# Kernel optimization log

Hardware: AMD Instinct MI355X
Metric: run time of the kernel (lower is better)

The kernel has to match this reference:

```python
import jax, jax.numpy as jnp
import numpy as np

D, H, DFF = 256, 8, 2048
NQ, BS, HW = 300, 16, 1444
HD = D // H

def _lin_params(key, din, dout):
    k1, k2 = jax.random.split(key)
    s = 1.0 / np.sqrt(din)
    W = jax.random.uniform(k1, (dout, din), minval=-s, maxval=s, dtype=jnp.float32)
    b = jax.random.uniform(k2, (dout,), minval=-s, maxval=s, dtype=jnp.float32)
    return W, b

def setup_inputs() -> dict:
    key = jax.random.key(0)
    ks = jax.random.split(key, 24)
    inp = {
        "tgt": jax.random.normal(ks[0], (NQ, BS, D), dtype=jnp.float32),
        "memory": jax.random.normal(ks[1], (HW, BS, D), dtype=jnp.float32),
        "pos": jax.random.normal(ks[2], (HW, BS, D), dtype=jnp.float32),
        "query_pos": jax.random.normal(ks[3], (NQ, BS, D), dtype=jnp.float32),
        "query_sine_embed": jax.random.normal(ks[4], (NQ, BS, D), dtype=jnp.float32),
        "memory_key_padding_mask": jnp.zeros((BS, HW), dtype=bool),
    }
    names = ["sa_qc", "sa_qp", "sa_kc", "sa_kp", "sa_v", "sa_out",
             "ca_qc", "ca_kc", "ca_kp", "ca_v", "ca_sine", "ca_out"]
    for i, n in enumerate(names):
        W, b = _lin_params(ks[5 + i], D, D)
        inp["W_" + n], inp["b_" + n] = W, b
    inp["W_ff1"], inp["b_ff1"] = _lin_params(ks[20], D, DFF)
    inp["W_ff2"], inp["b_ff2"] = _lin_params(ks[21], DFF, D)
    for n in ("n1", "n2", "n3"):
        inp["g_" + n] = jnp.ones((D,), jnp.float32)
        inp["be_" + n] = jnp.zeros((D,), jnp.float32)
    return inp

def _lin(x, W, b):
    return x @ W.T + b

def _ln(x, g, b):
    m = jnp.mean(x, axis=-1, keepdims=True)
    v = jnp.mean(jnp.square(x - m), axis=-1, keepdims=True)
    return (x - m) * jax.lax.rsqrt(v + 1e-5) * g + b

def reference(tgt, memory, pos, query_pos, query_sine_embed, memory_key_padding_mask,
              W_sa_qc, b_sa_qc, W_sa_qp, b_sa_qp, W_sa_kc, b_sa_kc, W_sa_kp, b_sa_kp,
              W_sa_v, b_sa_v, W_sa_out, b_sa_out,
              W_ca_qc, b_ca_qc, W_ca_kc, b_ca_kc, W_ca_kp, b_ca_kp, W_ca_v, b_ca_v,
              W_ca_sine, b_ca_sine, W_ca_out, b_ca_out,
              W_ff1, b_ff1, W_ff2, b_ff2,
              g_n1, be_n1, g_n2, be_n2, g_n3, be_n3):
    nq, bs, d = tgt.shape
    hw = memory.shape[0]
    # ---- self-attention (custom MHA: no internal in-proj, scale q, out_proj) ----
    q = _lin(tgt, W_sa_qc, b_sa_qc) + _lin(query_pos, W_sa_qp, b_sa_qp)
    k = _lin(tgt, W_sa_kc, b_sa_kc) + _lin(query_pos, W_sa_kp, b_sa_kp)
    v = _lin(tgt, W_sa_v, b_sa_v)
    qh = q.reshape(nq, bs, H, HD) * (HD ** -0.5)
    kh = k.reshape(nq, bs, H, HD)
    vh = v.reshape(nq, bs, H, HD)
    logits = jnp.einsum('qbhd,kbhd->bhqk', qh, kh)
    attn = jax.nn.softmax(logits, axis=-1)
    sa = jnp.einsum('bhqk,kbhd->qbhd', attn, vh).reshape(nq, bs, d)
    sa = _lin(sa, W_sa_out, b_sa_out)
    tgt = _ln(tgt + sa, g_n1, be_n1)
    # ---- cross-attention (is_first=False; concat content+pos per head -> 2d) ----
    qc = _lin(tgt, W_ca_qc, b_ca_qc)
    kc = _lin(memory, W_ca_kc, b_ca_kc)
    kp = _lin(pos, W_ca_kp, b_ca_kp)
    vm = _lin(memory, W_ca_v, b_ca_v)
    sine = _lin(query_sine_embed, W_ca_sine, b_ca_sine)
    qh2 = jnp.concatenate([qc.reshape(nq, bs, H, HD), sine.reshape(nq, bs, H, HD)], axis=-1)
    kh2 = jnp.concatenate([kc.reshape(hw, bs, H, HD), kp.reshape(hw, bs, H, HD)], axis=-1)
    vh2 = vm.reshape(hw, bs, H, HD)
    scale = (2 * HD) ** -0.5  # embed_dim of cross_attn is 2*d_model
    logits2 = jnp.einsum('qbhd,kbhd->bhqk', qh2 * scale, kh2)
    neg = jnp.finfo(logits2.dtype).min
    logits2 = jnp.where(memory_key_padding_mask[:, None, None, :], neg, logits2)
    attn2 = jax.nn.softmax(logits2, axis=-1)
    ca = jnp.einsum('bhqk,kbhd->qbhd', attn2, vh2).reshape(nq, bs, d)
    ca = _lin(ca, W_ca_out, b_ca_out)
    tgt = _ln(tgt + ca, g_n2, be_n2)
    # ---- FFN ----
    ff = _lin(jax.nn.relu(_lin(tgt, W_ff1, b_ff1)), W_ff2, b_ff2)
    return _ln(tgt + ff, g_n3, be_n3)
```

## Files before the change

### kernel.cpp

```cpp
#include <hip/hip_runtime.h>

typedef unsigned short u16;
typedef unsigned int u32;
typedef __attribute__((ext_vector_type(8))) short short8;
typedef __attribute__((ext_vector_type(4))) float f32x4;
typedef __attribute__((ext_vector_type(4))) unsigned short us4;

#define NQ 300
#define BS 16
#define HW 1444
#define DFF 2048
#define SA_TOK 4800
#define CA_TOK 23104

__device__ __forceinline__ float b2f(u16 x) {
    return __uint_as_float(((unsigned int)x) << 16);
}
__device__ __forceinline__ u16 f2b(float f) {
    unsigned int u = __float_as_uint(f);
    u += 0x7fffu + ((u >> 16) & 1u);
    return (u16)(u >> 16);
}

__device__ __forceinline__ int ext_mode(const void* dref) {
    const u16* p = (const u16*)dref;
    const int lane = threadIdx.x & 63;
    int hit = 0;
#pragma unroll
    for (int j = 0; j < 4; ++j) {
        u16 v = p[(lane * 4 + j) << 1];
        hit |= (((v >> 7) & 0xFF) >= 0xE0) ? 1 : 0;
    }
    unsigned long long b = __ballot(hit != 0);
    return (__popcll(b) >= 4) ? 1 : 0;
}

__device__ __forceinline__ float loadS(const void* p, size_t i, int m) {
    return m ? ((const float*)p)[i] : b2f(((const u16*)p)[i]);
}
__device__ __forceinline__ short8 load8(const void* p, size_t i, int m) {
    if (!m) return *(const short8*)((const u16*)p + i);
    const float* f = (const float*)p + i;
    float4 a = *(const float4*)f;
    float4 c = *(const float4*)(f + 4);
    short8 r;
    r[0] = (short)f2b(a.x); r[1] = (short)f2b(a.y);
    r[2] = (short)f2b(a.z); r[3] = (short)f2b(a.w);
    r[4] = (short)f2b(c.x); r[5] = (short)f2b(c.y);
    r[6] = (short)f2b(c.z); r[7] = (short)f2b(c.w);
    return r;
}

#define AW_SA_QC 0u
#define AW_SA_QP 65536u
#define AW_SA_KC 131072u
#define AW_SA_KP 196608u
#define AW_SA_V  262144u
#define AW_SA_O  327680u
#define AW_CA_QC 393216u
#define AW_CA_KC 458752u
#define AW_CA_KP 524288u
#define AW_CA_V  589824u
#define AW_CA_S  655360u
#define AW_CA_O  720896u
#define AW_FF1   786432u
#define AW_FF2   1310720u
#define AB_BASE  1835008u
#define AB_FF1   1838080u
#define AB_FF2   1840128u
#define AG_N1    1840384u
#define ABE_N1   1840640u
#define AG_N2    1840896u
#define ABE_N2   1841152u
#define AG_N3    1841408u
#define ABE_N3   1841664u

#define NPACK 34
struct PackDesc {
    const void* src[NPACK];
    u32 dst[NPACK];
    u32 cnt8[NPACK];
    u32 nd16[NPACK];
    u32 ksh[NPACK];
};

__global__ __launch_bounds__(256) void pack_kernel(PackDesc pd, u16* __restrict__ arena,
                                                   const void* __restrict__ dref)
{
    const int md = ext_mode(dref);
    const int ti = blockIdx.y;
    const void* src = pd.src[ti];
    const u32 dst = pd.dst[ti];
    const u32 n = pd.cnt8[ti];
    const u32 nd = pd.nd16[ti];
    if (nd) {
        const u32 ksh = pd.ksh[ti];
        const u32 kmask = (1u << ksh) - 1u;
        for (u32 c = blockIdx.x * 256 + threadIdx.x; c < n; c += gridDim.x * 256) {
            u32 e = c * 8;
            u32 nn = e >> ksh;
            u32 k = e & kmask;
            u32 d = ((k >> 5) * nd + (nn >> 4)) * 512 + (((k >> 3) & 3) * 16 + (nn & 15)) * 8;
            *(short8*)(arena + dst + d) = load8(src, (size_t)e, md);
        }
    } else {
        for (u32 c = blockIdx.x * 256 + threadIdx.x; c < n; c += gridDim.x * 256)
            *(short8*)(arena + dst + c * 8) = load8(src, (size_t)c * 8, md);
    }
}

__global__ __launch_bounds__(768, 3) void gemm_prod(
    const void* __restrict__ tgt, const void* __restrict__ qpos,
    const void* __restrict__ memory, const void* __restrict__ pos,
    const u16* __restrict__ arena,
    u16* __restrict__ Qb, u16* __restrict__ Kb, u16* __restrict__ Vb,
    u16* __restrict__ K2, u16* __restrict__ V2,
    float qscale, const void* __restrict__ dref)
{
    const int md = ext_mode(dref);
    __shared__ u16 AL[2 * 64 * 264];
    u16* A1 = AL;
    u16* A2 = AL + 64 * 264;
    const int tid = threadIdx.x;
    const int wave = tid >> 6, lane = tid & 63, quad = lane >> 4, l16 = lane & 15;

    if (blockIdx.x < 361) {
        const int m0 = blockIdx.x * 64;
#pragma unroll
        for (int i = 0; i < 6; ++i) {
            int c = tid + i * 768;
            if (c < 4096) {
                int t = c >> 11, local = c & 2047;
                int row = local >> 5, col = (local & 31) * 8;
                u16* A = t ? A2 : A1;
                const void* X = t ? pos : memory;
                *(short8*)(A + row * 264 + col) = load8(X, (size_t)(m0 + row) * 256 + col, md);
            }
        }
        __syncthreads();

        f32x4 acc[4][4];
#pragma unroll
        for (int rg = 0; rg < 4; ++rg)
#pragma unroll
            for (int s = 0; s < 4; ++s) acc[rg][s] = (f32x4){0,0,0,0};

        if (wave < 8) {
            const int h = wave;
            short8 bq[3][4];
#pragma unroll
            for (int p = 0; p < 2; ++p)
#pragma unroll
                for (int s = 0; s < 4; ++s) {
                    const u32 wo = (s < 2) ? AW_CA_KC : AW_CA_KP;
                    bq[p][s] = *(const short8*)(arena + wo + (u32)(p * 16 + h * 2 + (s & 1)) * 512 + lane * 8);
                }
#pragma unroll
            for (int i = 0; i < 8; ++i) {
                const int kk = i * 32;
                if (i < 6) {
#pragma unroll
                    for (int s = 0; s < 4; ++s) {
                        const u32 wo = (s < 2) ? AW_CA_KC : AW_CA_KP;
                        bq[(i + 2) % 3][s] = *(const short8*)(arena + wo + (u32)((i + 2) * 16 + h * 2 + (s & 1)) * 512 + lane * 8);
                    }
                }
                short8 am[4], ap[4];
#pragma unroll
                for (int rg = 0; rg < 4; ++rg) {
                    am[rg] = *(const short8*)(A1 + (rg * 16 + l16) * 264 + kk + quad * 8);
                    ap[rg] = *(const short8*)(A2 + (rg * 16 + l16) * 264 + kk + quad * 8);
                }
#pragma unroll
                for (int s = 0; s < 4; ++s)
#pragma unroll
                    for (int rg = 0; rg < 4; ++rg)
                        acc[rg][s] = __builtin_amdgcn_mfma_f32_16x16x32_bf16(
                            (s < 2) ? am[rg] : ap[rg], bq[i % 3][s], acc[rg][s], 0, 0, 0);
            }
        } else {
            const int nt = (wave - 8) * 4;
            short8 bq[3][4];
#pragma unroll
            for (int p = 0; p < 2; ++p)
#pragma unroll
                for (int s = 0; s < 4; ++s)
                    bq[p][s] = *(const short8*)(arena + AW_CA_V + (u32)(p * 16 + nt + s) * 512 + lane * 8);
#pragma unroll
            for (int i = 0; i < 8; ++i) {
                const int kk = i * 32;
                if (i < 6) {
#pragma unroll
                    for (int s = 0; s < 4; ++s)
                        bq[(i + 2) % 3][s] = *(const short8*)(arena + AW_CA_V + (u32)((i + 2) * 16 + nt + s) * 512 + lane * 8);
                }
                short8 am[4];
#pragma unroll
                for (int rg = 0; rg < 4; ++rg)
                    am[rg] = *(const short8*)(A1 + (rg * 16 + l16) * 264 + kk + quad * 8);
#pragma unroll
                for (int s = 0; s < 4; ++s)
#pragma unroll
                    for (int rg = 0; rg < 4; ++rg)
                        acc[rg][s] = __builtin_amdgcn_mfma_f32_16x16x32_bf16(am[rg], bq[i % 3][s], acc[rg][s], 0, 0, 0);
            }
        }

        __syncthreads();
        if (wave < 8) {
            const int h = wave;
#pragma unroll
            for (int s = 0; s < 4; ++s) {
                const int brow = h * 32 + (s & 1) * 16 + l16;
                float bv = b2f(arena[((s < 2) ? (AB_BASE + 7 * 256) : (AB_BASE + 8 * 256)) + brow]);
                const int col = h * 64 + s * 16 + l16;
#pragma unroll
                for (int rg = 0; rg < 4; ++rg)
#pragma unroll
                    for (int r = 0; r < 4; ++r)
                        AL[(rg * 16 + quad * 4 + r) * 520 + col] = f2b(acc[rg][s][r] + bv);
            }
        }
        __syncthreads();
        for (int c = tid; c < 4096; c += 768) {
            int row = c >> 6, cc = (c & 63) * 8;
            *(short8*)(K2 + (size_t)(m0 + row) * 512 + cc) = *(const short8*)(AL + row * 520 + cc);
        }
        __syncthreads();
        if (wave >= 8) {
            const int n0 = (wave - 8) * 64;
#pragma unroll
            for (int s = 0; s < 4; ++s) {
                const int col = n0 + s * 16 + l16;
                float bv = b2f(arena[AB_BASE + 9 * 256 + col]);
#pragma unroll
                for (int rg = 0; rg < 4; ++rg)
#pragma unroll
                    for (int r = 0; r < 4; ++r)
                        AL[(rg * 16 + quad * 4 + r) * 264 + col] = f2b(acc[rg][s][r] + bv);
            }
        }
        __syncthreads();
        for (int c = tid; c < 2048; c += 768) {
            int row = c >> 5, cc = (c & 31) * 8;
            *(short8*)(V2 + (size_t)(m0 + row) * 256 + cc) = *(const short8*)(AL + row * 264 + cc);
        }
    } else {
        const int m0 = (blockIdx.x - 361) * 64;
#pragma unroll
        for (int i = 0; i < 6; ++i) {
            int c = tid + i * 768;
            if (c < 4096) {
                int t = c >> 11, local = c & 2047;
                int row = local >> 5, col = (local & 31) * 8;
                u16* A = t ? A2 : A1;
                const void* X = t ? qpos : tgt;
                *(short8*)(A + row * 264 + col) = load8(X, (size_t)(m0 + row) * 256 + col, md);
            }
        }
        __syncthreads();

        const int grp = wave >> 2, sub = wave & 3;
        const int n0 = sub * 64, nt = sub * 4;
        u32 w1o, w2o, b1o, b2o; int dual; float scale;
        if (grp == 0)      { w1o = AW_SA_QC; w2o = AW_SA_QP; b1o = AB_BASE;         b2o = AB_BASE + 256;   dual = 1; scale = qscale; }
        else if (grp == 1) { w1o = AW_SA_KC; w2o = AW_SA_KP; b1o = AB_BASE + 512;   b2o = AB_BASE + 768;   dual = 1; scale = 1.f;    }
        else               { w1o = AW_SA_V;  w2o = 0;        b1o = AB_BASE + 1024;  b2o = 0;               dual = 0; scale = 1.f;    }

        f32x4 acc[4][4];
#pragma unroll
        for (int rg = 0; rg < 4; ++rg)
#pragma unroll
            for (int s = 0; s < 4; ++s) acc[rg][s] = (f32x4){0,0,0,0};

        {
            short8 bw[3][4];
#pragma unroll
            for (int p = 0; p < 2; ++p)
#pragma unroll
                for (int s = 0; s < 4; ++s)
                    bw[p][s] = *(const short8*)(arena + w1o + (u32)(p * 16 + nt + s) * 512 + lane * 8);
#pragma unroll
            for (int i = 0; i < 8; ++i) {
                const int kk = i * 32;
                if (i < 6) {
#pragma unroll
                    for (int s = 0; s < 4; ++s)
                        bw[(i + 2) % 3][s] = *(const short8*)(arena + w1o + (u32)((i + 2) * 16 + nt + s) * 512 + lane * 8);
                }
                short8 a[4];
#pragma unroll
                for (int rg = 0; rg < 4; ++rg)
                    a[rg] = *(const short8*)(A1 + (rg * 16 + l16) * 264 + kk + quad * 8);
#pragma unroll
                for (int s = 0; s < 4; ++s)
#pragma unroll
                    for (int rg = 0; rg < 4; ++rg)
                        acc[rg][s] = __builtin_amdgcn_mfma_f32_16x16x32_bf16(a[rg], bw[i % 3][s], acc[rg][s], 0, 0, 0);
            }
        }
        if (dual) {
            short8 bw[3][4];
#pragma unroll
            for (int p = 0; p < 2; ++p)
#pragma unroll
                for (int s = 0; s < 4; ++s)
                    bw[p][s] = *(const short8*)(arena + w2o + (u32)(p * 16 + nt + s) * 512 + lane * 8);
#pragma unroll
            for (int i = 0; i < 8; ++i) {
                const int kk = i * 32;
                if (i < 6) {
#pragma unroll
                    for (int s = 0; s < 4; ++s)
                        bw[(i + 2) % 3][s] = *(const short8*)(arena + w2o + (u32)((i + 2) * 16 + nt + s) * 512 + lane * 8);
                }
                short8 a[4];
#pragma unroll
                for (int rg = 0; rg < 4; ++rg)
                    a[rg] = *(const short8*)(A2 + (rg * 16 + l16) * 264 + kk + quad * 8);
#pragma unroll
                for (int s = 0; s < 4; ++s)
#pragma unroll
                    for (int rg = 0; rg < 4; ++rg)
                        acc[rg][s] = __builtin_amdgcn_mfma_f32_16x16x32_bf16(a[rg], bw[i % 3][s], acc[rg][s], 0, 0, 0);
            }
        }

        __syncthreads();
        if (grp < 2) {
#pragma unroll
            for (int s = 0; s < 4; ++s) {
                const int col = n0 + s * 16 + l16;
                float bv = b2f(arena[b1o + col]);
                if (dual) bv += b2f(arena[b2o + col]);
#pragma unroll
                for (int rg = 0; rg < 4; ++rg)
#pragma unroll
                    for (int r = 0; r < 4; ++r)
                        AL[grp * (64 * 264) + (rg * 16 + quad * 4 + r) * 264 + col] = f2b((acc[rg][s][r] + bv) * scale);
            }
        }
        __syncthreads();
#pragma unroll
        for (int i = 0; i < 6; ++i) {
            int c = tid + i * 768;
            if (c < 4096) {
                int t = c >> 11, local = c & 2047;
                int row = local >> 5, cc = (local & 31) * 8;
                u16* Y = t ? Kb : Qb;
                *(short8*)(Y + (size_t)(m0 + row) * 256 + cc) =
                    *(const short8*)(AL + t * (64 * 264) + row * 264 + cc);
            }
        }
        __syncthreads();
        if (grp == 2) {
#pragma unroll
            for (int s = 0; s < 4; ++s) {
                const int col = n0 + s * 16 + l16;
                float bv = b2f(arena[b1o + col]);
#pragma unroll
                for (int rg = 0; rg < 4; ++rg)
#pragma unroll
                    for (int r = 0; r < 4; ++r)
                        AL[(rg * 16 + quad * 4 + r) * 264 + col] = f2b(acc[rg][s][r] + bv);
            }
        }
        __syncthreads();
#pragma unroll
        for (int i = 0; i < 3; ++i) {
            int c = tid + i * 768;
            if (c < 2048) {
                int row = c >> 5, cc = (c & 31) * 8;
                *(short8*)(Vb + (size_t)(m0 + row) * 256 + cc) = *(const short8*)(AL + row * 264 + cc);
            }
        }
    }
}

__global__ __launch_bounds__(256) void gemm_ff1(
    const u16* __restrict__ X, const u16* __restrict__ arena,
    u16* __restrict__ Y)
{
    __shared__ u16 A[64 * 264];
    const int tid = threadIdx.x;
    const int m0 = blockIdx.x * 64;
    for (int c = tid; c < 2048; c += 256) {
        int row = c >> 5, col = (c & 31) * 8;
        *(short8*)(A + row * 264 + col) = *(const short8*)(X + (size_t)(m0 + row) * 256 + col);
    }
    __syncthreads();

    const int wave = tid >> 6, lane = tid & 63, quad = lane >> 4, l16 = lane & 15;
    const int n0 = (blockIdx.y * 4 + wave) * 64;
    const u32 nt = (u32)(n0 >> 4);
    f32x4 acc[4][4];
#pragma unroll
    for (int rg = 0; rg < 4; ++rg)
#pragma unroll
        for (int s = 0; s < 4; ++s) acc[rg][s] = (f32x4){0,0,0,0};

    short8 bw[3][4];
#pragma unroll
    for (int p = 0; p < 2; ++p)
#pragma unroll
        for (int s = 0; s < 4; ++s)
            bw[p][s] = *(const short8*)(arena + AW_FF1 + (u32)(p * 128 + nt + s) * 512 + lane * 8);
#pragma unroll
    for (int i = 0; i < 8; ++i) {
        const int kk = i * 32;
        if (i < 6) {
#pragma unroll
            for (int s = 0; s < 4; ++s)
                bw[(i + 2) % 3][s] = *(const short8*)(arena + AW_FF1 + (u32)((i + 2) * 128 + nt + s) * 512 + lane * 8);
        }
        short8 a[4];
#pragma unroll
        for (int rg = 0; rg < 4; ++rg)
            a[rg] = *(const short8*)(A + (rg * 16 + l16) * 264 + kk + quad * 8);
#pragma unroll
        for (int s = 0; s < 4; ++s)
#pragma unroll
            for (int rg = 0; rg < 4; ++rg)
                acc[rg][s] = __builtin_amdgcn_mfma_f32_16x16x32_bf16(a[rg], bw[i % 3][s], acc[rg][s], 0, 0, 0);
    }

    __syncthreads();
    const int lcol = wave * 64;
#pragma unroll
    for (int s = 0; s < 4; ++s) {
        const int col = n0 + s * 16 + l16;
        float bv = b2f(arena[AB_FF1 + col]);
#pragma unroll
        for (int rg = 0; rg < 4; ++rg)
#pragma unroll
            for (int r = 0; r < 4; ++r) {
                float v = fmaxf(acc[rg][s][r] + bv, 0.f);
                A[(rg * 16 + quad * 4 + r) * 264 + lcol + s * 16 + l16] = f2b(v);
            }
    }
    __syncthreads();
    const size_t cbase = (size_t)blockIdx.y * 256;
    for (int c = tid; c < 2048; c += 256) {
        int row = c >> 5, cc = (c & 31) * 8;
        *(short8*)(Y + (size_t)(m0 + row) * 2048 + cbase + cc) = *(const short8*)(A + row * 264 + cc);
    }
}

__global__ __launch_bounds__(256) void gemm_ln(
    const u16* __restrict__ X, const u16* __restrict__ arena,
    u32 wo, u32 bo, u32 go, u32 beo,
    const void* __restrict__ R, int rext,
    u16* __restrict__ Out, const void* __restrict__ dref)
{
    const int md = ext_mode(dref);
    const int mr = rext ? md : 0;
    __shared__ u16 A[32 * 264];
    __shared__ float S[32][260];
    const int tid = threadIdx.x;
    const int m0 = blockIdx.x * 32;
    for (int c = tid; c < 1024; c += 256) {
        int row = c >> 5, col = (c & 31) * 8;
        *(short8*)(A + row * 264 + col) = *(const short8*)(X + (size_t)(m0 + row) * 256 + col);
    }
    __syncthreads();

    const int wave = tid >> 6, lane = tid & 63, quad = lane >> 4, l16 = lane & 15;
    const int n0 = wave * 64;
    const u32 nt = (u32)(wave * 4);
    f32x4 acc[2][4];
#pragma unroll
    for (int rg = 0; rg < 2; ++rg)
#pragma unroll
        for (int s = 0; s < 4; ++s) acc[rg][s] = (f32x4){0,0,0,0};

    short8 bw[4][4];
#pragma unroll
    for (int p = 0; p < 3; ++p)
#pragma unroll
        for (int s = 0; s < 4; ++s)
            bw[p][s] = *(const short8*)(arena + wo + (u32)(p * 16 + nt + s) * 512 + lane * 8);
#pragma unroll
    for (int i = 0; i < 8; ++i) {
        const int kk = i * 32;
        if (i < 5) {
#pragma unroll
            for (int s = 0; s < 4; ++s)
                bw[(i + 3) & 3][s] = *(const short8*)(arena + wo + (u32)((i + 3) * 16 + nt + s) * 512 + lane * 8);
        }
        short8 a0 = *(const short8*)(A + l16 * 264 + kk + quad * 8);
        short8 a1 = *(const short8*)(A + (16 + l16) * 264 + kk + quad * 8);
#pragma unroll
        for (int s = 0; s < 4; ++s) {
            acc[0][s] = __builtin_amdgcn_mfma_f32_16x16x32_bf16(a0, bw[i & 3][s], acc[0][s], 0, 0, 0);
            acc[1][s] = __builtin_amdgcn_mfma_f32_16x16x32_bf16(a1, bw[i & 3][s], acc[1][s], 0, 0, 0);
        }
    }
#pragma unroll
    for (int s = 0; s < 4; ++s) {
        const int col = n0 + s * 16 + l16;
        float bv = b2f(arena[bo + col]);
#pragma unroll
        for (int rg = 0; rg < 2; ++rg)
#pragma unroll
            for (int r = 0; r < 4; ++r)
                S[rg * 16 + quad * 4 + r][col] = acc[rg][s][r] + bv;
    }
    __syncthreads();

#pragma unroll
    for (int rr = 0; rr < 8; ++rr) {
        const int row = wave * 8 + rr;
        float4 v = *(const float4*)&S[row][lane * 4];
        const size_t rb = (size_t)(m0 + row) * 256 + lane * 4;
        v.x += loadS(R, rb + 0, mr);
        v.y += loadS(R, rb + 1, mr);
        v.z += loadS(R, rb + 2, mr);
        v.w += loadS(R, rb + 3, mr);
        float s = v.x + v.y + v.z + v.w;
        float q = v.x * v.x + v.y * v.y + v.z * v.z + v.w * v.w;
#pragma unroll
        for (int off = 1; off <= 32; off <<= 1) {
            s += __shfl_xor(s, off);
            q += __shfl_xor(q, off);
        }
        const float mean = s * (1.f / 256.f);
        const float var  = q * (1.f / 256.f) - mean * mean;
        const float rs   = rsqrtf(var + 1e-5f);
        float vv[4] = {v.x, v.y, v.z, v.w};
        us4 ov;
#pragma unroll
        for (int j = 0; j < 4; ++j) {
            const int col = lane * 4 + j;
            float o = (vv[j] - mean) * rs * b2f(arena[go + col]) + b2f(arena[beo + col]);
            ov[j] = f2b(o);
        }
        *(us4*)(Out + (size_t)(m0 + row) * 256 + lane * 4) = ov;
    }
}

__global__ __launch_bounds__(512) void gemm_cat(
    const void* __restrict__ Xa, int xae, const void* __restrict__ Xb, int xbe,
    const u16* __restrict__ arena, u32 wao, u32 wbo, u32 bao, u32 bbo,
    u16* __restrict__ Y, float scale, const void* __restrict__ dref)
{
    const int md = ext_mode(dref);
    __shared__ u16 AL[2 * 32 * 264];
    u16* Aa = AL;
    u16* Ab = AL + 32 * 264;
    const int tid = threadIdx.x;
    const int m0 = blockIdx.x * 32;
    for (int c = tid; c < 2048; c += 512) {
        const int t = c >> 10, local = c & 1023;
        const int row = local >> 5, col = (local & 31) * 8;
        const void* X = t ? Xb : Xa;
        const int xfp = (t ? xbe : xae) ? md : 0;
        u16* A = t ? Ab : Aa;
        *(short8*)(A + row * 264 + col) = load8(X, (size_t)(m0 + row) * 256 + col, xfp);
    }
    __syncthreads();

    const int wave = tid >> 6, lane = tid & 63, quad = lane >> 4, l16 = lane & 15;
    const int h = wave;
    f32x4 acc[2][4];
#pragma unroll
    for (int rg = 0; rg < 2; ++rg)
#pragma unroll
        for (int s = 0; s < 4; ++s) acc[rg][s] = (f32x4){0,0,0,0};

    short8 bw[4][4];
#pragma unroll
    for (int p = 0; p < 3; ++p)
#pragma unroll
        for (int s = 0; s < 4; ++s) {
            const u32 wo = (s < 2) ? wao : wbo;
            bw[p][s] = *(const short8*)(arena + wo + (u32)(p * 16 + h * 2 + (s & 1)) * 512 + lane * 8);
        }
#pragma unroll
    for (int i = 0; i < 8; ++i) {
        const int kk = i * 32;
        if (i < 5) {
#pragma unroll
            for (int s = 0; s < 4; ++s) {
                const u32 wo = (s < 2) ? wao : wbo;
                bw[(i + 3) & 3][s] = *(const short8*)(arena + wo + (u32)((i + 3) * 16 + h * 2 + (s & 1)) * 512 + lane * 8);
            }
        }
        short8 aa[2], ab[2];
#pragma unroll
        for (int rg = 0; rg < 2; ++rg) {
            aa[rg] = *(const short8*)(Aa + (rg * 16 + l16) * 264 + kk + quad * 8);
            ab[rg] = *(const short8*)(Ab + (rg * 16 + l16) * 264 + kk + quad * 8);
        }
#pragma unroll
        for (int s = 0; s < 4; ++s)
#pragma unroll
            for (int rg = 0; rg < 2; ++rg)
                acc[rg][s] = __builtin_amdgcn_mfma_f32_16x16x32_bf16(
                    (s < 2) ? aa[rg] : ab[rg], bw[i & 3][s], acc[rg][s], 0, 0, 0);
    }

    __syncthreads();
#pragma unroll
    for (int s = 0; s < 4; ++s) {
        const int brow = h * 32 + (s & 1) * 16 + l16;
        float bv = b2f(arena[((s < 2) ? bao : bbo) + brow]);
        const int col = h * 64 + s * 16 + l16;
#pragma unroll
        for (int rg = 0; rg < 2; ++rg)
#pragma unroll
            for (int r = 0; r < 4; ++r)
                AL[(rg * 16 + quad * 4 + r) * 520 + col] = f2b((acc[rg][s][r] + bv) * scale);
    }
    __syncthreads();
    for (int c = tid; c < 2048; c += 512) {
        int row = c >> 6, cc = (c & 63) * 8;
        *(short8*)(Y + (size_t)(m0 + row) * 512 + cc) = *(const short8*)(AL + row * 520 + cc);
    }
}

__global__ __launch_bounds__(256) void gemm_ff2s(
    const u16* __restrict__ X, const u16* __restrict__ arena, u32 wo,
    u16* __restrict__ P)
{
    __shared__ u16 A[64 * 520];
    const int tid = threadIdx.x;
    const int m0 = blockIdx.x * 64;
    const int ks = blockIdx.y;
    const int kbase = ks * 512;
    for (int c = tid; c < 4096; c += 256) {
        int row = c >> 6, col = (c & 63) * 8;
        *(short8*)(A + row * 520 + col) =
            *(const short8*)(X + (size_t)(m0 + row) * 2048 + kbase + col);
    }
    __syncthreads();

    const int wave = tid >> 6, lane = tid & 63, quad = lane >> 4, l16 = lane & 15;
    const int n0 = wave * 64;
    const u32 nt = (u32)(wave * 4);
    const u32 kt0 = (u32)(ks * 16);
    f32x4 acc[4][4];
#pragma unroll
    for (int rg = 0; rg < 4; ++rg)
#pragma unroll
        for (int s = 0; s < 4; ++s) acc[rg][s] = (f32x4){0,0,0,0};

    short8 bw[3][4];
#pragma unroll
    for (int p = 0; p < 2; ++p)
#pragma unroll
        for (int s = 0; s < 4; ++s)
            bw[p][s] = *(const short8*)(arena + wo + ((kt0 + p) * 16 + nt + s) * 512 + lane * 8);
#pragma unroll
    for (int i = 0; i < 16; ++i) {
        const int kk = i * 32;
        if (i < 14) {
#pragma unroll
            for (int s = 0; s < 4; ++s)
                bw[(i + 2) % 3][s] = *(const short8*)(arena + wo + ((kt0 + i + 2) * 16 + nt + s) * 512 + lane * 8);
        }
        short8 a[4];
#pragma unroll
        for (int rg = 0; rg < 4; ++rg)
            a[rg] = *(const short8*)(A + (rg * 16 + l16) * 520 + kk + quad * 8);
#pragma unroll
        for (int s = 0; s < 4; ++s)
#pragma unroll
            for (int rg = 0; rg < 4; ++rg)
                acc[rg][s] = __builtin_amdgcn_mfma_f32_16x16x32_bf16(a[rg], bw[i % 3][s], acc[rg][s], 0, 0, 0);
    }

    __syncthreads();
#pragma unroll
    for (int s = 0; s < 4; ++s) {
        const int col = n0 + s * 16 + l16;
#pragma unroll
        for (int rg = 0; rg < 4; ++rg)
#pragma unroll
            for (int r = 0; r < 4; ++r)
                A[(rg * 16 + quad * 4 + r) * 264 + col] = f2b(acc[rg][s][r]);
    }
    __syncthreads();
    for (int c = tid; c < 2048; c += 256) {
        int row = c >> 5, cc = (c & 31) * 8;
        *(short8*)(P + ((size_t)ks * SA_TOK + m0 + row) * 256 + cc) = *(const short8*)(A + row * 264 + cc);
    }
}

__global__ __launch_bounds__(256) void ln_ff2(
    const u16* __restrict__ P, const u16* __restrict__ arena,
    u32 bo, u32 go, u32 beo, const u16* __restrict__ T2,
    void* __restrict__ Out, const void* __restrict__ dref)
{
    const int md = ext_mode(dref);
    const int t = blockIdx.x;
    const int i = threadIdx.x;
    const int lane = i & 63, wave = i >> 6;
    float v = b2f(arena[bo + i]) + b2f(T2[(size_t)t * 256 + i]);
#pragma unroll
    for (int ks = 0; ks < 4; ++ks)
        v += b2f(P[((size_t)ks * SA_TOK + t) * 256 + i]);

    __shared__ float ssum[4], ssq[4];
    float s = v, q = v * v;
#pragma unroll
    for (int off = 32; off >= 1; off >>= 1) {
        s += __shfl_down(s, off, 64);
        q += __shfl_down(q, off, 64);
    }
    if (lane == 0) { ssum[wave] = s; ssq[wave] = q; }
    __syncthreads();
    float mean = (ssum[0] + ssum[1] + ssum[2] + ssum[3]) * (1.f / 256.f);
    float var  = (ssq[0] + ssq[1] + ssq[2] + ssq[3]) * (1.f / 256.f) - mean * mean;
    float o = (v - mean) * rsqrtf(var + 1e-5f) * b2f(arena[go + i]) + b2f(arena[beo + i]);
    const size_t oi = (size_t)t * 256 + i;
    if (md) ((float*)Out)[oi] = o;
    else    ((u16*)Out)[oi]   = f2b(o);
}

__global__ __launch_bounds__(256) void zero_f4(float4* __restrict__ p, u32 n4)
{
    u32 i = blockIdx.x * 256 + threadIdx.x;
    if (i < n4) p[i] = (float4){0.f, 0.f, 0.f, 0.f};
}

template <int KD>
__global__ __launch_bounds__(256) void attn_es(
    const u16* __restrict__ Qb, const u16* __restrict__ Kb,
    const u16* __restrict__ Vb, u16* __restrict__ Ob, int nk, int klen,
    float* __restrict__ Po, float* __restrict__ Pl)
{
    const int QS  = (KD == 32) ? 256 : 512;
    const int KDS = KD + 8;
    const int NF  = KD / 32;
    __shared__ u16 lds[64 * (KD + 8) + 32 * 72 + 4 * 16 * 72];
    u16* Kt = lds;
    u16* Vt = lds + 64 * KDS;
    u16* Pb = Vt + 32 * 72;

    const int tid = threadIdx.x;
    const int wave = tid >> 6, lane = tid & 63, quad = lane >> 4, l16 = lane & 15;
    u16* Pw = Pb + wave * 16 * 72;

    const int bh = blockIdx.x, b = bh >> 3, h = bh & 7;
    const int kbeg = blockIdx.z * klen;
    const int kend = (kbeg + klen < nk) ? (kbeg + klen) : nk;
    const int qt = blockIdx.y * 64 + wave * 16;
    const int qi = qt + l16;
    const int qc = (qi < NQ) ? qi : (NQ - 1);

    short8 qf[NF];
#pragma unroll
    for (int f = 0; f < NF; ++f)
        qf[f] = *(const short8*)(Qb + (size_t)(qc * BS + b) * QS + h * KD + f * 32 + quad * 8);

    f32x4 o0 = {0,0,0,0}, o1 = {0,0,0,0};
    float lsum = 0.f;

    short8 rk[NF];
    us4 rv[2];
#pragma unroll
    for (int j = 0; j < NF; ++j) {
        int idx = j * 256 + tid, key = idx / (KD / 8), dc = (idx % (KD / 8)) * 8;
        int kk = kbeg + key; if (kk >= kend) kk = kend - 1;
        rk[j] = *(const short8*)(Kb + (size_t)(kk * BS + b) * QS + h * KD + dc);
    }
#pragma unroll
    for (int j = 0; j < 2; ++j) {
        int idx = j * 256 + tid, key = idx & 63, g = idx >> 6;
        int kk = kbeg + key; if (kk >= kend) kk = kend - 1;
        rv[j] = *(const us4*)(Vb + (size_t)(kk * BS + b) * 256 + h * 32 + g * 4);
    }

    for (int k0 = kbeg; k0 < kend; k0 += 64) {
        __syncthreads();
#pragma unroll
        for (int j = 0; j < NF; ++j) {
            int idx = j * 256 + tid, key = idx / (KD / 8), dc = (idx % (KD / 8)) * 8;
            *(short8*)(Kt + key * KDS + dc) = rk[j];
        }
#pragma unroll
        for (int j = 0; j < 2; ++j) {
            int idx = j * 256 + tid, key = idx & 63, g = idx >> 6;
#pragma unroll
            for (int i2 = 0; i2 < 4; ++i2) Vt[(g * 4 + i2) * 72 + key] = rv[j][i2];
        }
        __syncthreads();
        if (k0 + 64 < kend) {
#pragma unroll
            for (int j = 0; j < NF; ++j) {
                int idx = j * 256 + tid, key = idx / (KD / 8), dc = (idx % (KD / 8)) * 8;
                int kk = k0 + 64 + key; if (kk >= kend) kk = kend - 1;
                rk[j] = *(const short8*)(Kb + (size_t)(kk * BS + b) * QS + h * KD + dc);
            }
#pragma unroll
            for (int j = 0; j < 2; ++j) {
                int idx = j * 256 + tid, key = idx & 63, g = idx >> 6;
                int kk = k0 + 64 + key; if (kk >= kend) kk = kend - 1;
                rv[j] = *(const us4*)(Vb + (size_t)(kk * BS + b) * 256 + h * 32 + g * 4);
            }
        }

#pragma unroll
        for (int t = 0; t < 4; ++t) {
            f32x4 c = {0,0,0,0};
#pragma unroll
            for (int f = 0; f < NF; ++f) {
                short8 a = *(const short8*)(Kt + (t * 16 + l16) * KDS + f * 32 + quad * 8);
                c = __builtin_amdgcn_mfma_f32_16x16x32_bf16(a, qf[f], c, 0, 0, 0);
            }
            float pv[4];
#pragma unroll
            for (int r = 0; r < 4; ++r) {
                int keyg = k0 + t * 16 + quad * 4 + r;
                float p = (keyg < kend) ? __expf(fminf(c[r], 60.f)) : 0.f;
                pv[r] = p; lsum += p;
            }
            uint2 pk;
            pk.x = (u32)f2b(pv[0]) | ((u32)f2b(pv[1]) << 16);
            pk.y = (u32)f2b(pv[2]) | ((u32)f2b(pv[3]) << 16);
            *(uint2*)(Pw + l16 * 72 + t * 16 + quad * 4) = pk;
        }
        short8 ap0 = *(const short8*)(Pw + l16 * 72 + quad * 8);
        short8 ap1 = *(const short8*)(Pw + l16 * 72 + 32 + quad * 8);
        short8 b00 = *(const short8*)(Vt + l16 * 72 + quad * 8);
        short8 b01 = *(const short8*)(Vt + l16 * 72 + 32 + quad * 8);
        short8 b10 = *(const short8*)(Vt + (16 + l16) * 72 + quad * 8);
        short8 b11 = *(const short8*)(Vt + (16 + l16) * 72 + 32 + quad * 8);
        o0 = __builtin_amdgcn_mfma_f32_16x16x32_bf16(ap0, b00, o0, 0, 0, 0);
        o0 = __builtin_amdgcn_mfma_f32_16x16x32_bf16(ap1, b01, o0, 0, 0, 0);
        o1 = __builtin_amdgcn_mfma_f32_16x16x32_bf16(ap0, b10, o1, 0, 0, 0);
        o1 = __builtin_amdgcn_mfma_f32_16x16x32_bf16(ap1, b11, o1, 0, 0, 0);
    }

    lsum += __shfl_xor(lsum, 16);
    lsum += __shfl_xor(lsum, 32);
    if (Po) {
#pragma unroll
        for (int r = 0; r < 4; ++r) {
            const int q = qt + quad * 4 + r;
            if (q < NQ) {
                float* op = Po + (size_t)(q * BS + b) * 256 + h * 32;
                atomicAdd(op + l16, o0[r]);
                atomicAdd(op + 16 + l16, o1[r]);
            }
        }
        if (quad == 0 && qi < NQ)
            atomicAdd(Pl + (size_t)(qi * BS + b) * 8 + h, lsum);
    } else {
#pragma unroll
        for (int r = 0; r < 4; ++r) {
            const int qlocal = quad * 4 + r;
            float lr = __shfl(lsum, (lane & 48) + qlocal);
            const int q = qt + qlocal;
            if (q < NQ) {
                float inv = 1.f / lr;
                u16* op = Ob + (size_t)(q * BS + b) * 256 + h * 32;
                op[l16]      = f2b(o0[r] * inv);
                op[16 + l16] = f2b(o1[r] * inv);
            }
        }
    }
}

__global__ __launch_bounds__(256) void attn_comb(
    const float* __restrict__ Po, const float* __restrict__ Pl,
    u16* __restrict__ Ob)
{
    const int t = blockIdx.x;
    const int i = threadIdx.x;
    float v = Po[(size_t)t * 256 + i];
    float l = Pl[t * 8 + (i >> 5)];
    Ob[(size_t)t * 256 + i] = f2b(v / l);
}

#define O_ARENA ((size_t)0)
#define O_T1    ((size_t)1841920)
#define O_AT    ((size_t)3070720)
#define O_QB    ((size_t)4299520)
#define O_KB    ((size_t)5528320)
#define O_VB    ((size_t)6757120)
#define O_Q2    ((size_t)7985920)
#define O_K2    ((size_t)10443520)
#define O_V2    ((size_t)22272768)
#define O_T2    ((size_t)28187392)
#define O_FF1   O_K2
#define O_FF2P  O_AT

extern "C" void kernel_launch(void* const* d_in, const int* in_sizes, int n_in,
                              void* d_out, int out_size, void* d_ws, size_t ws_size,
                              hipStream_t stream)
{
    const void* tgt    = d_in[0];
    const void* memory = d_in[1];
    const void* pos    = d_in[2];
    const void* qpos   = d_in[3];
    const void* qsine  = d_in[4];

    u16* ws = (u16*)d_ws;
    u16* arena = ws + O_ARENA;
    u16* T1   = ws + O_T1;
    u16* ATb  = ws + O_AT;
    u16* Qb   = ws + O_QB;
    u16* Kb   = ws + O_KB;
    u16* Vb   = ws + O_VB;
    u16* Q2   = ws + O_Q2;
    u16* K2   = ws + O_K2;
    u16* V2   = ws + O_V2;
    u16* T2   = ws + O_T2;
    u16* FF1  = ws + O_FF1;
    u16* FF2P = ws + O_AT;
    float* Po = (float*)(ws + O_QB);
    float* Pl = (float*)(ws + O_VB);

    PackDesc pd;
    static const u32 sizes[NPACK] = {
        65536,65536,65536,65536,65536,65536,
        65536,65536,65536,65536,65536,65536,
        524288,524288,
        256,256,256,256,256,256,
        256,256,256,256,256,256,
        2048,256,
        256,256,256,256,256,256 };
    static const u32 nd16a[NPACK] = {
        16,16,16,16,16,16,
        16,16,16,16,16,16,
        128,16,
        0,0,0,0,0,0,
        0,0,0,0,0,0,
        0,0,
        0,0,0,0,0,0 };
    static const u32 ksha[NPACK] = {
        8,8,8,8,8,8,
        8,8,8,8,8,8,
        8,11,
        0,0,0,0,0,0,
        0,0,0,0,0,0,
        0,0,
        0,0,0,0,0,0 };
    int wi[14] = {6,8,10,12,14,16,18,20,22,24,26,28,30,32};
    for (int i = 0; i < 14; ++i) pd.src[i] = d_in[wi[i]];
    for (int i = 0; i < 14; ++i) pd.src[14 + i] = d_in[wi[i] + 1];
    for (int i = 0; i < 6; ++i)  pd.src[28 + i] = d_in[34 + i];
    u32 off = 0;
    for (int i = 0; i < NPACK; ++i) {
        pd.dst[i] = off; pd.cnt8[i] = sizes[i] / 8;
        pd.nd16[i] = nd16a[i]; pd.ksh[i] = ksha[i];
        off += sizes[i];
    }

    const float sa_scale = 0.17677669529663689f;
    const float ca_scale = 0.125f;

    pack_kernel<<<dim3(128, NPACK), 256, 0, stream>>>(pd, arena, tgt);

    gemm_prod<<<436, 768, 0, stream>>>(tgt, qpos, memory, pos, arena,
        Qb, Kb, Vb, K2, V2, sa_scale, tgt);

    attn_es<32><<<dim3(128, 5, 1), 256, 0, stream>>>(Qb, Kb, Vb, ATb, NQ, NQ,
        nullptr, nullptr);
    zero_f4<<<1800, 256, 0, stream>>>((float4*)(ws + O_QB), 460800u);
    gemm_ln<<<150, 256, 0, stream>>>(ATb, arena, AW_SA_O, AB_BASE + 5*256,
        AG_N1, ABE_N1, tgt, 1, T1, tgt);

    gemm_cat<<<150, 512, 0, stream>>>(T1, 0, qsine, 1, arena,
        AW_CA_QC, AW_CA_S, AB_BASE + 6*256, AB_BASE + 10*256, Q2, ca_scale, tgt);
    attn_es<64><<<dim3(128, 5, 4), 256, 0, stream>>>(Q2, K2, V2, ATb, HW, 361,
        Po, Pl);
    attn_comb<<<SA_TOK, 256, 0, stream>>>(Po, Pl, ATb);
    gemm_ln<<<150, 256, 0, stream>>>(ATb, arena, AW_CA_O, AB_BASE + 11*256,
        AG_N2, ABE_N2, T1, 0, T2, tgt);

    gemm_ff1<<<dim3(75, 8), 256, 0, stream>>>(T2, arena, FF1);
    gemm_ff2s<<<dim3(75, 4), 256, 0, stream>>>(FF1, arena, AW_FF2, FF2P);
    ln_ff2<<<SA_TOK, 256, 0, stream>>>(FF2P, arena, AB_FF2, AG_N3, ABE_N3,
        T2, d_out, tgt);
}
```

Measured before the change: 333.3 us.

## Fuse attention split-K combine into gemm_ln and split self-attention keys

Removes the separate attn_comb kernel by having gemm_ln read the fp32 partial outputs and row sums and normalise them while loading its A tile. Self-attention now also splits its keys into two chunks (grid z=2, klen 150), accumulating through the same atomic partial-sum path to give more blocks. The zeroing kernel handles both the output and sum buffers, and a second zeroing launch is added for the self-attention buffers. The trade-offs are extra atomics and fp32 traffic for self-attention, and one more launch.

```diff
diff --git a/kernel.cpp b/kernel.cpp
--- a/kernel.cpp
+++ b/kernel.cpp
@@ -450,7 +450,8 @@
     const u16* __restrict__ X, const u16* __restrict__ arena,
     u32 wo, u32 bo, u32 go, u32 beo,
     const void* __restrict__ R, int rext,
-    u16* __restrict__ Out, const void* __restrict__ dref)
+    u16* __restrict__ Out, const void* __restrict__ dref,
+    const float* __restrict__ Po, const float* __restrict__ Pl)
 {
     const int md = ext_mode(dref);
     const int mr = rext ? md : 0;
@@ -458,9 +459,26 @@
     __shared__ float S[32][260];
     const int tid = threadIdx.x;
     const int m0 = blockIdx.x * 32;
-    for (int c = tid; c < 1024; c += 256) {
-        int row = c >> 5, col = (c & 31) * 8;
-        *(short8*)(A + row * 264 + col) = *(const short8*)(X + (size_t)(m0 + row) * 256 + col);
+    if (Po) {
+        for (int c = tid; c < 1024; c += 256) {
+            int row = c >> 5, col = (c & 31) * 8;
+            int token = m0 + row;
+            const float* src = Po + (size_t)token * 256 + col;
+            float4 a = *(const float4*)src;
+            float4 b4 = *(const float4*)(src + 4);
+            float inv = 1.f / Pl[token * 8 + (col >> 5)];
+            short8 r;
+            r[0] = (short)f2b(a.x * inv); r[1] = (short)f2b(a.y * inv);
+            r[2] = (short)f2b(a.z * inv); r[3] = (short)f2b(a.w * inv);
+            r[4] = (short)f2b(b4.x * inv); r[5] = (short)f2b(b4.y * inv);
+            r[6] = (short)f2b(b4.z * inv); r[7] = (short)f2b(b4.w * inv);
+            *(short8*)(A + row * 264 + col) = r;
+        }
+    } else {
+        for (int c = tid; c < 1024; c += 256) {
+            int row = c >> 5, col = (c & 31) * 8;
+            *(short8*)(A + row * 264 + col) = *(const short8*)(X + (size_t)(m0 + row) * 256 + col);
+        }
     }
     __syncthreads();
 
@@ -717,10 +735,12 @@
     else    ((u16*)Out)[oi]   = f2b(o);
 }
 
-__global__ __launch_bounds__(256) void zero_f4(float4* __restrict__ p, u32 n4)
+__global__ __launch_bounds__(256) void zero2(
+    float4* __restrict__ a, u32 na, float4* __restrict__ b, u32 nb)
 {
     u32 i = blockIdx.x * 256 + threadIdx.x;
-    if (i < n4) p[i] = (float4){0.f, 0.f, 0.f, 0.f};
+    if (i < na) a[i] = (float4){0.f, 0.f, 0.f, 0.f};
+    else if (i - na < nb) b[i - na] = (float4){0.f, 0.f, 0.f, 0.f};
 }
 
 template <int KD>
@@ -862,17 +882,6 @@
     }
 }
 
-__global__ __launch_bounds__(256) void attn_comb(
-    const float* __restrict__ Po, const float* __restrict__ Pl,
-    u16* __restrict__ Ob)
-{
-    const int t = blockIdx.x;
-    const int i = threadIdx.x;
-    float v = Po[(size_t)t * 256 + i];
-    float l = Pl[t * 8 + (i >> 5)];
-    Ob[(size_t)t * 256 + i] = f2b(v / l);
-}
-
 #define O_ARENA ((size_t)0)
 #define O_T1    ((size_t)1841920)
 #define O_AT    ((size_t)3070720)
@@ -899,7 +908,6 @@
     u16* ws = (u16*)d_ws;
     u16* arena = ws + O_ARENA;
     u16* T1   = ws + O_T1;
-    u16* ATb  = ws + O_AT;
     u16* Qb   = ws + O_QB;
     u16* Kb   = ws + O_KB;
     u16* Vb   = ws + O_VB;
@@ -909,8 +917,10 @@
     u16* T2   = ws + O_T2;
     u16* FF1  = ws + O_FF1;
     u16* FF2P = ws + O_AT;
-    float* Po = (float*)(ws + O_QB);
-    float* Pl = (float*)(ws + O_VB);
+    float* PoCA = (float*)(ws + O_QB);
+    float* PlCA = (float*)(ws + O_VB);
+    float* PoSA = (float*)(ws + O_Q2);
+    float* PlSA = (float*)(ws + O_AT);
 
     PackDesc pd;
     static const u32 sizes[NPACK] = {
@@ -952,23 +962,23 @@
     const float ca_scale = 0.125f;
 
     pack_kernel<<<dim3(128, NPACK), 256, 0, stream>>>(pd, arena, tgt);
+    zero2<<<1238, 256, 0, stream>>>((float4*)PoSA, 307200u, (float4*)PlSA, 9600u);
 
     gemm_prod<<<436, 768, 0, stream>>>(tgt, qpos, memory, pos, arena,
         Qb, Kb, Vb, K2, V2, sa_scale, tgt);
 
-    attn_es<32><<<dim3(128, 5, 1), 256, 0, stream>>>(Qb, Kb, Vb, ATb, NQ, NQ,
-        nullptr, nullptr);
-    zero_f4<<<1800, 256, 0, stream>>>((float4*)(ws + O_QB), 460800u);
-    gemm_ln<<<150, 256, 0, stream>>>(ATb, arena, AW_SA_O, AB_BASE + 5*256,
-        AG_N1, ABE_N1, tgt, 1, T1, tgt);
+    attn_es<32><<<dim3(128, 5, 2), 256, 0, stream>>>(Qb, Kb, Vb, nullptr, NQ, 150,
+        PoSA, PlSA);
+    zero2<<<1238, 256, 0, stream>>>((float4*)PoCA, 307200u, (float4*)PlCA, 9600u);
+    gemm_ln<<<150, 256, 0, stream>>>(nullptr, arena, AW_SA_O, AB_BASE + 5*256,
+        AG_N1, ABE_N1, tgt, 1, T1, tgt, PoSA, PlSA);
 
     gemm_cat<<<150, 512, 0, stream>>>(T1, 0, qsine, 1, arena,
         AW_CA_QC, AW_CA_S, AB_BASE + 6*256, AB_BASE + 10*256, Q2, ca_scale, tgt);
-    attn_es<64><<<dim3(128, 5, 4), 256, 0, stream>>>(Q2, K2, V2, ATb, HW, 361,
-        Po, Pl);
-    attn_comb<<<SA_TOK, 256, 0, stream>>>(Po, Pl, ATb);
-    gemm_ln<<<150, 256, 0, stream>>>(ATb, arena, AW_CA_O, AB_BASE + 11*256,
-        AG_N2, ABE_N2, T1, 0, T2, tgt);
+    attn_es<64><<<dim3(128, 5, 4), 256, 0, stream>>>(Q2, K2, V2, nullptr, HW, 361,
+        PoCA, PlCA);
+    gemm_ln<<<150, 256, 0, stream>>>(nullptr, arena, AW_CA_O, AB_BASE + 11*256,
+        AG_N2, ABE_N2, T1, 0, T2, tgt, PoCA, PlCA);
 
     gemm_ff1<<<dim3(75, 8), 256, 0, stream>>>(T2, arena, FF1);
     gemm_ff2s<<<dim3(75, 4), 256, 0, stream>>>(FF1, arena, AW_FF2, FF2P);
```

Result: slower. 343.1 us (+2.9%).
